# Kernel optimization log

Measured on AMD Instinct MI355X. Metric: run time of the kernel, lower is better.

## Reference

```python
import jax, jax.numpy as jnp
import numpy as np

B, N, D, H = 8, 128, 768, 64
NEG = -1e30
SLOPE = 0.01  # LeakyReLU slope
EPS = 1e-5    # BatchNorm eps


def setup_inputs() -> dict:
    key = jax.random.key(0)
    ks = jax.random.split(key, 10)
    s = 0.02
    feature = jax.random.normal(ks[0], (B, N, D), jnp.float32)
    aspect = jax.random.normal(ks[1], (B, D), jnp.float32)
    adj = jax.random.randint(ks[2], (B, N, N), 0, 2).astype(jnp.int32)
    W0 = jax.random.normal(ks[3], (D, D), jnp.float32) * s
    b0 = jnp.zeros((D,), jnp.float32)
    W1 = jax.random.normal(ks[4], (D, D), jnp.float32) * s
    b1 = jnp.zeros((D,), jnp.float32)
    A1 = jax.random.normal(ks[5], (2 * D, H), jnp.float32) * s  # afcs[0]
    ab1 = jnp.zeros((H,), jnp.float32)
    A2 = jax.random.normal(ks[6], (H, 1), jnp.float32) * s      # afcs[2]
    ab2 = jnp.zeros((1,), jnp.float32)
    gamma = jnp.ones((D,), jnp.float32)
    beta = jnp.zeros((D,), jnp.float32)
    return dict(feature=feature, aspect=aspect, adj=adj, W0=W0, b0=b0,
                W1=W1, b1=b1, A1=A1, ab1=ab1, A2=A2, ab2=ab2,
                gamma=gamma, beta=beta)


def reference(feature, aspect, adj, W0, b0, W1, b1, A1, ab1, A2, ab2, gamma, beta):
    # aspect is unused by the original forward.
    m = adj.astype(feature.dtype)          # [B,N,N] 0/1 mask
    d = A1.shape[0] // 2
    A1s, A1t = A1[:d], A1[d:]              # weight-split of Linear(2*mem_dim, H):
                                           # [h_i, h_j] @ A1 == h_i @ A1s + h_j @ A1t
    for (W, b) in ((W0, b0), (W1, b1)):
        h = feature @ W + b                # [B,N,D]
        s_src = h @ A1s                    # [B,N,H], broadcast over j
        s_tgt = h @ A1t                    # [B,N,H], broadcast over i
        hid = jax.nn.relu(s_src[:, :, None, :] + s_tgt[:, None, :, :] + ab1)  # [B,N,N,H]
        e = (hid @ A2)[..., 0] + ab2[0]    # [B,N,N]
        e = jnp.where(e > 0, e, SLOPE * e)  # LeakyReLU(0.01)
        logits = e * m + (1.0 - m) * NEG    # mask_logits
        b_, n_ = logits.shape[0], logits.shape[1]
        # NOTE: original softmaxes over the FLATTENED N*N axis, not per-row.
        attn = jax.nn.softmax(logits.reshape(b_, n_ * n_), axis=-1).reshape(b_, n_, n_)
        feature = jnp.einsum('bij,bjd->bid', attn, h)  # attention.bmm(h)
        # dropout is identity in eval / deterministic reference
    node_feature = feature
    g = node_feature.sum(axis=1)           # [B,D]
    mean = g.mean(axis=0)
    var = g.var(axis=0)                    # biased, matches BN training forward
    graph_feature = gamma * (g - mean) / jnp.sqrt(var + EPS) + beta
    return graph_feature, node_feature
```

## Files before the change

### kernel.cpp

```cpp
#include <hip/hip_runtime.h>
#include <math.h>

#define NEG_V (-1e30f)
#define SLOPE_V 0.01f
#define EPS_V 1e-5f

typedef __attribute__((ext_vector_type(8))) short bs8;
typedef __attribute__((ext_vector_type(4))) float f32x4;


__device__ __forceinline__ void split2(float x, unsigned short& hi, unsigned short& lo) {
    unsigned u = __float_as_uint(x);
    unsigned h = (u + 0x7FFFu + ((u >> 16) & 1u)) >> 16;
    hi = (unsigned short)h;
    float hf = __uint_as_float(h << 16);
    float l = x - hf;
    unsigned ul = __float_as_uint(l);
    lo = (unsigned short)((ul + 0x7FFFu + ((ul >> 16) & 1u)) >> 16);
}

#define MFMA_COMPUTE(B0)                                                       \
    {                                                                          \
        bs8 a_h[2], a_l[2], b_h[2], b_l[2];                                    \
        _Pragma("unroll")                                                      \
        for (int t = 0; t < 2; t++) {                                          \
            a_h[t] = *(bs8*)&buf[(B0) + 0][wm0 + t * 16 + lm][q * 8];          \
            a_l[t] = *(bs8*)&buf[(B0) + 1][wm0 + t * 16 + lm][q * 8];          \
            b_h[t] = *(bs8*)&buf[(B0) + 2][wn0 + t * 16 + lm][q * 8];          \
            b_l[t] = *(bs8*)&buf[(B0) + 3][wn0 + t * 16 + lm][q * 8];          \
        }                                                                      \
        _Pragma("unroll")                                                      \
        for (int mt = 0; mt < 2; mt++)                                         \
            _Pragma("unroll")                                                  \
            for (int nt = 0; nt < 2; nt++) {                                   \
                acc[mt][nt] = __builtin_amdgcn_mfma_f32_16x16x32_bf16(a_h[mt], b_h[nt], acc[mt][nt], 0, 0, 0); \
                acc[mt][nt] = __builtin_amdgcn_mfma_f32_16x16x32_bf16(a_h[mt], b_l[nt], acc[mt][nt], 0, 0, 0); \
                acc[mt][nt] = __builtin_amdgcn_mfma_f32_16x16x32_bf16(a_l[mt], b_h[nt], acc[mt][nt], 0, 0, 0); \
            }                                                                  \
    }

__device__ __forceinline__ void mfma_loop(
    const unsigned short* __restrict__ Ahg, const unsigned short* __restrict__ Alg,
    int lda,
    const unsigned short* __restrict__ Bhg, const unsigned short* __restrict__ Blg,
    int ldb, int K, int row0, int col0,
    f32x4 (&acc)[2][2],
    unsigned short (*buf)[64][40])
{
    const int tid = threadIdx.x;
    const int lane = tid & 63, wid = tid >> 6;
    const int wm0 = (wid >> 1) * 32, wn0 = (wid & 1) * 32;
    const int lm = lane & 15, q = lane >> 4;
    const int sr = tid >> 2, sc = (tid & 3) * 8;

    const unsigned short* pAh = Ahg + (size_t)(row0 + sr) * lda + sc;
    const unsigned short* pAl = Alg + (size_t)(row0 + sr) * lda + sc;
    const unsigned short* pBh = Bhg + (size_t)(col0 + sr) * ldb + sc;
    const unsigned short* pBl = Blg + (size_t)(col0 + sr) * ldb + sc;

    bs8 xAh = *(const bs8*)(pAh);
    bs8 xAl = *(const bs8*)(pAl);
    bs8 xBh = *(const bs8*)(pBh);
    bs8 xBl = *(const bs8*)(pBl);
    bs8 yAh = *(const bs8*)(pAh + 32);
    bs8 yAl = *(const bs8*)(pAl + 32);
    bs8 yBh = *(const bs8*)(pBh + 32);
    bs8 yBl = *(const bs8*)(pBl + 32);

    for (int k0 = 0; k0 < K; k0 += 64) {
        *(bs8*)&buf[0][sr][sc] = xAh;
        *(bs8*)&buf[1][sr][sc] = xAl;
        *(bs8*)&buf[2][sr][sc] = xBh;
        *(bs8*)&buf[3][sr][sc] = xBl;
        __syncthreads();
        if (k0 + 64 < K) {
            xAh = *(const bs8*)(pAh + k0 + 64);
            xAl = *(const bs8*)(pAl + k0 + 64);
            xBh = *(const bs8*)(pBh + k0 + 64);
            xBl = *(const bs8*)(pBl + k0 + 64);
        }
        MFMA_COMPUTE(0);
        *(bs8*)&buf[4][sr][sc] = yAh;
        *(bs8*)&buf[5][sr][sc] = yAl;
        *(bs8*)&buf[6][sr][sc] = yBh;
        *(bs8*)&buf[7][sr][sc] = yBl;
        __syncthreads();
        if (k0 + 96 < K) {
            yAh = *(const bs8*)(pAh + k0 + 96);
            yAl = *(const bs8*)(pAl + k0 + 96);
            yBh = *(const bs8*)(pBh + k0 + 96);
            yBl = *(const bs8*)(pBl + k0 + 96);
        }
        MFMA_COMPUTE(4);
    }
}

__device__ __forceinline__ void transpose_split_tile(
    const float* __restrict__ src, int src_ld,
    unsigned short* __restrict__ dh, unsigned short* __restrict__ dl, int dst_ld,
    unsigned short (*Th)[72], unsigned short (*Tl)[72])
{
    int tid = threadIdx.x;
    int r = tid >> 2;
    int cb = (tid & 3) * 16;
#pragma unroll
    for (int cc = 0; cc < 16; cc += 4) {
        float4 v = *(const float4*)(src + (size_t)r * src_ld + cb + cc);
        unsigned short hh, ll;
        split2(v.x, hh, ll); Th[cb + cc + 0][r] = hh; Tl[cb + cc + 0][r] = ll;
        split2(v.y, hh, ll); Th[cb + cc + 1][r] = hh; Tl[cb + cc + 1][r] = ll;
        split2(v.z, hh, ll); Th[cb + cc + 2][r] = hh; Tl[cb + cc + 2][r] = ll;
        split2(v.w, hh, ll); Th[cb + cc + 3][r] = hh; Tl[cb + cc + 3][r] = ll;
    }
    __syncthreads();
    int n = tid >> 2, ch = (tid & 3) * 8;
    *(bs8*)(dh + (size_t)n * dst_ld + ch)      = *(bs8*)&Th[n][ch];
    *(bs8*)(dh + (size_t)n * dst_ld + ch + 32) = *(bs8*)&Th[n][ch + 32];
    *(bs8*)(dl + (size_t)n * dst_ld + ch)      = *(bs8*)&Tl[n][ch];
    *(bs8*)(dl + (size_t)n * dst_ld + ch + 32) = *(bs8*)&Tl[n][ch + 32];
}

__device__ __forceinline__ void flat_split_job(
    const float* __restrict__ src, unsigned short* __restrict__ dh,
    unsigned short* __restrict__ dl, size_t base)
{
    unsigned short hh, ll;
#pragma unroll
    for (int g = 0; g < 2; g++) {
        bs8 sh, sl;
#pragma unroll
        for (int cc = 0; cc < 8; cc += 4) {
            float4 v = *(const float4*)(src + base + g * 8 + cc);
            split2(v.x, hh, ll); sh[cc + 0] = (short)hh; sl[cc + 0] = (short)ll;
            split2(v.y, hh, ll); sh[cc + 1] = (short)hh; sl[cc + 1] = (short)ll;
            split2(v.z, hh, ll); sh[cc + 2] = (short)hh; sl[cc + 2] = (short)ll;
            split2(v.w, hh, ll); sh[cc + 3] = (short)hh; sl[cc + 3] = (short)ll;
        }
        *(bs8*)(dh + base + g * 8) = sh;
        *(bs8*)(dl + base + g * 8) = sl;
    }
}

#define WA_STORE(va0, va1, vw0, vw1) {                                       \
    unsigned short hv, lv;                                                   \
    split2((va0).x, hv, lv); Ah[acs + 0][akk] = hv; Al[acs + 0][akk] = lv;   \
    split2((va0).y, hv, lv); Ah[acs + 1][akk] = hv; Al[acs + 1][akk] = lv;   \
    split2((va0).z, hv, lv); Ah[acs + 2][akk] = hv; Al[acs + 2][akk] = lv;   \
    split2((va0).w, hv, lv); Ah[acs + 3][akk] = hv; Al[acs + 3][akk] = lv;   \
    split2((va1).x, hv, lv); Ah[acs + 4][akk] = hv; Al[acs + 4][akk] = lv;   \
    split2((va1).y, hv, lv); Ah[acs + 5][akk] = hv; Al[acs + 5][akk] = lv;   \
    split2((va1).z, hv, lv); Ah[acs + 6][akk] = hv; Al[acs + 6][akk] = lv;   \
    split2((va1).w, hv, lv); Ah[acs + 7][akk] = hv; Al[acs + 7][akk] = lv;   \
    bs8 sh, sl;                                                              \
    split2((vw0).x, hv, lv); sh[0] = (short)hv; sl[0] = (short)lv;           \
    split2((vw0).y, hv, lv); sh[1] = (short)hv; sl[1] = (short)lv;           \
    split2((vw0).z, hv, lv); sh[2] = (short)hv; sl[2] = (short)lv;           \
    split2((vw0).w, hv, lv); sh[3] = (short)hv; sl[3] = (short)lv;           \
    split2((vw1).x, hv, lv); sh[4] = (short)hv; sl[4] = (short)lv;           \
    split2((vw1).y, hv, lv); sh[5] = (short)hv; sl[5] = (short)lv;           \
    split2((vw1).z, hv, lv); sh[6] = (short)hv; sl[6] = (short)lv;           \
    split2((vw1).w, hv, lv); sh[7] = (short)hv; sl[7] = (short)lv;           \
    *(bs8*)&Bh[br][bks] = sh;                                                \
    *(bs8*)&Bl[br][bks] = sl;                                                \
}

#define WA_FRAG() {                                                          \
    bs8 a_h[2], a_l[2], b_h[2], b_l[2];                                      \
    _Pragma("unroll")                                                        \
    for (int t = 0; t < 2; t++) {                                            \
        a_h[t] = *(bs8*)&Ah[wm0 + t * 16 + lm][q * 8];                       \
        a_l[t] = *(bs8*)&Al[wm0 + t * 16 + lm][q * 8];                       \
        b_h[t] = *(bs8*)&Bh[wn0 + t * 16 + lm][q * 8];                       \
        b_l[t] = *(bs8*)&Bl[wn0 + t * 16 + lm][q * 8];                       \
    }                                                                        \
    _Pragma("unroll")                                                        \
    for (int mt = 0; mt < 2; mt++)                                           \
        _Pragma("unroll")                                                    \
        for (int nt = 0; nt < 2; nt++) {                                     \
            acc[mt][nt] = __builtin_amdgcn_mfma_f32_16x16x32_bf16(a_h[mt], b_h[nt], acc[mt][nt], 0, 0, 0); \
            acc[mt][nt] = __builtin_amdgcn_mfma_f32_16x16x32_bf16(a_h[mt], b_l[nt], acc[mt][nt], 0, 0, 0); \
            acc[mt][nt] = __builtin_amdgcn_mfma_f32_16x16x32_bf16(a_l[mt], b_h[nt], acc[mt][nt], 0, 0, 0); \
        }                                                                    \
}

__global__ __launch_bounds__(256) void prep_k(
    const float* __restrict__ W0, const float* __restrict__ W1,
    const float* __restrict__ A1, const float* __restrict__ feature,
    const float* __restrict__ b0, const float* __restrict__ b1,
    unsigned short* Wt0h, unsigned short* Wt0l,
    unsigned short* Wt1h, unsigned short* Wt1l,
    unsigned short* fh, unsigned short* fl,
    unsigned short* WAth, unsigned short* WAtl,
    float* bA)
{
    __shared__ __align__(16) char smem[20480];
    int id = blockIdx.x, tid = threadIdx.x;
    if (id < 288) {
        unsigned short (*Th)[72] = (unsigned short(*)[72])(smem);
        unsigned short (*Tl)[72] = (unsigned short(*)[72])(smem + 9216);
        if (id < 144) {
            int kt = id / 12, nt = id % 12;
            transpose_split_tile(W0 + (size_t)(kt * 64) * 768 + nt * 64, 768,
                                 Wt0h + (size_t)(nt * 64) * 768 + kt * 64,
                                 Wt0l + (size_t)(nt * 64) * 768 + kt * 64, 768, Th, Tl);
        } else {
            int r = id - 144, kt = r / 12, nt = r % 12;
            transpose_split_tile(W1 + (size_t)(kt * 64) * 768 + nt * 64, 768,
                                 Wt1h + (size_t)(nt * 64) * 768 + kt * 64,
                                 Wt1l + (size_t)(nt * 64) * 768 + kt * 64, 768, Th, Tl);
        }
    } else if (id < 480) {
        flat_split_job(feature, fh, fl, (size_t)(id - 288) * 4096 + tid * 16);
    } else if (id < 528) {
        int j = id - 480;
        int c8 = j & 7, kq8 = j >> 3;
        int layer = (c8 >> 1) & 1;
        int ct = c8 & 1;
        int rt = kq8 + 6 * (c8 >> 2);
        const float* W = layer ? W1 : W0;
        const int r0 = rt * 64;
        unsigned short (*Ah)[40] = (unsigned short(*)[40])(smem);
        unsigned short (*Al)[40] = (unsigned short(*)[40])(smem + 5120);
        unsigned short (*Bh)[40] = (unsigned short(*)[40])(smem + 10240);
        unsigned short (*Bl)[40] = (unsigned short(*)[40])(smem + 15360);
        const int lane = tid & 63, wid = tid >> 6;
        const int wm0 = (wid >> 1) * 32, wn0 = (wid & 1) * 32;
        const int lm = lane & 15, q = lane >> 4;
        const int akk = tid & 31, acs = (tid >> 5) * 8;
        const int br = tid >> 2, bks = (tid & 3) * 8;
        const float* A1p = A1 + (size_t)(ct * 768 + akk) * 64 + acs;
        const float* Wp  = W + (size_t)(r0 + br) * 768 + bks;
        float4 xa0 = *(const float4*)(A1p);
        float4 xa1 = *(const float4*)(A1p + 4);
        float4 xw0 = *(const float4*)(Wp);
        float4 xw1 = *(const float4*)(Wp + 4);
        float4 ya0 = *(const float4*)(A1p + 32 * 64);
        float4 ya1 = *(const float4*)(A1p + 32 * 64 + 4);
        float4 yw0 = *(const float4*)(Wp + 32);
        float4 yw1 = *(const float4*)(Wp + 36);
        f32x4 acc[2][2] = {};
        for (int k0 = 0; k0 < 768; k0 += 64) {
            WA_STORE(xa0, xa1, xw0, xw1);
            __syncthreads();
            if (k0 + 64 < 768) {
                xa0 = *(const float4*)(A1p + (size_t)(k0 + 64) * 64);
                xa1 = *(const float4*)(A1p + (size_t)(k0 + 64) * 64 + 4);
                xw0 = *(const float4*)(Wp + k0 + 64);
                xw1 = *(const float4*)(Wp + k0 + 68);
            }
            WA_FRAG();
            __syncthreads();
            WA_STORE(ya0, ya1, yw0, yw1);
            __syncthreads();
            if (k0 + 96 < 768) {
                ya0 = *(const float4*)(A1p + (size_t)(k0 + 96) * 64);
                ya1 = *(const float4*)(A1p + (size_t)(k0 + 96) * 64 + 4);
                yw0 = *(const float4*)(Wp + k0 + 96);
                yw1 = *(const float4*)(Wp + k0 + 100);
            }
            WA_FRAG();
            __syncthreads();
        }
        const int c0 = ct * 64;
        size_t base = (size_t)layer * 98304;
#pragma unroll
        for (int mt = 0; mt < 2; mt++)
#pragma unroll
            for (int nt = 0; nt < 2; nt++) {
                int n = r0 + wn0 + nt * 16 + lm;
#pragma unroll
                for (int i = 0; i < 4; i++) {
                    int m = c0 + wm0 + mt * 16 + q * 4 + i;
                    unsigned short hv, lv;
                    split2(acc[mt][nt][i], hv, lv);
                    WAth[base + (size_t)m * 768 + n] = hv;
                    WAtl[base + (size_t)m * 768 + n] = lv;
                }
            }
    } else {
        float* redb = (float*)(smem);
        int layer = id - 528;
        const float* bv = layer ? b1 : b0;
        int c = tid & 127, half = tid >> 7;
        float acc = 0.f;
        for (int kk = 0; kk < 384; kk++) {
            int k = half * 384 + kk;
            int row = (c < 64 ? k : 768 + k);
            acc += bv[k] * A1[(size_t)row * 64 + (c & 63)];
        }
        redb[tid] = acc;
        __syncthreads();
        if (tid < 128) bA[layer * 128 + tid] = redb[tid] + redb[tid + 128];
    }
}

__global__ __launch_bounds__(256) void gemm_fused_k(
    const unsigned short* __restrict__ Ahg, const unsigned short* __restrict__ Alg,
    const unsigned short* __restrict__ Wth, const unsigned short* __restrict__ Wtl,
    const unsigned short* __restrict__ WAth, const unsigned short* __restrict__ WAtl,
    const float* __restrict__ bias,
    unsigned short* __restrict__ hth, unsigned short* __restrict__ htl,
    float* __restrict__ s)
{
    __shared__ unsigned short smem[8][64][40];
    int id = blockIdx.x;
    int g = id >> 3, r8 = id & 7;
    int hi2 = (g >= 14) ? 1 : 0;
    int by = r8 + 8 * hi2;
    int bx = g - 14 * hi2;
    int row0 = by * 64;
    const unsigned short* Bh;
    const unsigned short* Bl;
    int col0;
    if (bx < 12) { Bh = Wth;  Bl = Wtl;  col0 = bx * 64; }
    else         { Bh = WAth; Bl = WAtl; col0 = (bx - 12) * 64; }
    f32x4 acc[2][2] = {};
    mfma_loop(Ahg, Alg, 768, Bh, Bl, 768, 768, row0, col0, acc, smem);
    int tid = threadIdx.x, lane = tid & 63, wid = tid >> 6;
    int wm0 = (wid >> 1) * 32, wn0 = (wid & 1) * 32;
    int lm = lane & 15, q = lane >> 4;
    if (bx >= 12) {
#pragma unroll
        for (int mt = 0; mt < 2; mt++)
#pragma unroll
            for (int nt = 0; nt < 2; nt++) {
                int c = col0 + wn0 + nt * 16 + lm;
#pragma unroll
                for (int i = 0; i < 4; i++) {
                    int r = row0 + wm0 + mt * 16 + q * 4 + i;
                    s[(size_t)r * 128 + c] = acc[mt][nt][i];
                }
            }
        return;
    }
    __syncthreads();
    unsigned short* flat = &smem[0][0][0];
    unsigned short (*Hi)[69] = (unsigned short(*)[69])flat;
    unsigned short (*Lo)[69] = (unsigned short(*)[69])(flat + 4416);
#pragma unroll
    for (int mt = 0; mt < 2; mt++)
#pragma unroll
        for (int nt = 0; nt < 2; nt++) {
            int c = wn0 + nt * 16 + lm;
            float bv = bias[col0 + c];
#pragma unroll
            for (int i = 0; i < 4; i++) {
                int r = wm0 + mt * 16 + q * 4 + i;
                unsigned short hv, lv;
                split2(acc[mt][nt][i] + bv, hv, lv);
                Hi[r][c] = hv; Lo[r][c] = lv;
            }
        }
    __syncthreads();
    int d = tid >> 2, kq = (tid & 3) * 16;
    int b = row0 >> 7, kb = row0 & 127;
    bs8 th0, th1, tl0, tl1;
#pragma unroll
    for (int e = 0; e < 8; e++) {
        th0[e] = Hi[kq + e][d];     th1[e] = Hi[kq + 8 + e][d];
        tl0[e] = Lo[kq + e][d];     tl1[e] = Lo[kq + 8 + e][d];
    }
    size_t to = ((size_t)b * 768 + col0 + d) * 128 + kb + kq;
    *(bs8*)(hth + to) = th0; *(bs8*)(hth + to + 8) = th1;
    *(bs8*)(htl + to) = tl0; *(bs8*)(htl + to + 8) = tl1;
}

__global__ __launch_bounds__(256) void score_k(
    const float* __restrict__ s, const int* __restrict__ adj,
    const float* __restrict__ ab1, const float* __restrict__ A2,
    const float* __restrict__ ab2, const float* __restrict__ bA,
    unsigned short* __restrict__ ph, unsigned short* __restrict__ pl,
    float* __restrict__ psum)
{
    __shared__ float st[128][65];
    __shared__ float ss[4][65];
    __shared__ float a2s[64];
    __shared__ float warr[4];
    const int id = blockIdx.x, tid = threadIdx.x;
    const int b = id & 7, bx = id >> 3;
    const int i0 = bx * 4;
#pragma unroll
    for (int g = 0; g < 8; g++) {
        int idx4 = tid + g * 256;
        int j = idx4 >> 4;
        int h2 = (idx4 & 15) * 4;
        float4 v = *(const float4*)&s[(size_t)(b * 128 + j) * 128 + 64 + h2];
        float4 bv = *(const float4*)&bA[64 + h2];
        st[j][h2 + 0] = v.x + bv.x;
        st[j][h2 + 1] = v.y + bv.y;
        st[j][h2 + 2] = v.z + bv.z;
        st[j][h2 + 3] = v.w + bv.w;
    }
    {
        int i = tid >> 6, h2 = tid & 63;
        ss[i][h2] = s[(size_t)(b * 128 + i0 + i) * 128 + h2] + bA[h2] + ab1[h2];
    }
    if (tid < 64) a2s[tid] = A2[tid];
    __syncthreads();
    const float ab2v = ab2[0];
    const int rr = tid >> 7;
    const int j = tid & 127;
    const int r0 = rr * 2, r1 = rr * 2 + 1;
    float acc0 = 0.f, acc1 = 0.f;
#pragma unroll 4
    for (int h2 = 0; h2 < 64; h2++) {
        float bb = st[j][h2];
        float cv = a2s[h2];
        acc0 = fmaf(fmaxf(ss[r0][h2] + bb, 0.f), cv, acc0);
        acc1 = fmaf(fmaxf(ss[r1][h2] + bb, 0.f), cv, acc1);
    }
    float e0 = acc0 + ab2v; e0 = (e0 > 0.f) ? e0 : SLOPE_V * e0;
    float e1 = acc1 + ab2v; e1 = (e1 > 0.f) ? e1 : SLOPE_V * e1;
    size_t o0 = (size_t)b * 16384 + (size_t)(i0 + r0) * 128 + j;
    size_t o1 = (size_t)b * 16384 + (size_t)(i0 + r1) * 128 + j;
    float v0 = adj[o0] ? expf(e0) : 0.f;
    float v1 = adj[o1] ? expf(e1) : 0.f;
    unsigned short hv, lv;
    split2(v0, hv, lv); ph[o0] = hv; pl[o0] = lv;
    split2(v1, hv, lv); ph[o1] = hv; pl[o1] = lv;
    float vs = v0 + v1;
#pragma unroll
    for (int o = 32; o > 0; o >>= 1) vs += __shfl_down(vs, o);
    if ((tid & 63) == 0) warr[tid >> 6] = vs;
    __syncthreads();
    if (tid == 0) psum[b * 32 + bx] = warr[0] + warr[1] + warr[2] + warr[3];
}

__global__ __launch_bounds__(256) void attn_mfma_k(
    const unsigned short* __restrict__ ph, const unsigned short* __restrict__ pl,
    const unsigned short* __restrict__ hth, const unsigned short* __restrict__ htl,
    const float* __restrict__ psum, float* __restrict__ node,
    unsigned short* __restrict__ nodeh, unsigned short* __restrict__ nodel)
{
    __shared__ unsigned short smem[8][64][40];
    __shared__ float sred[33];
    int id = blockIdx.x;
    int b = id & 7, t = id >> 3;
    int cx = t % 12, ry = t / 12;
    int row0 = ry * 64, col0 = cx * 64;
    int tid = threadIdx.x;
    if (tid < 32) sred[tid] = psum[b * 32 + tid];
    __syncthreads();
    if (tid == 0) {
        float tt = 0.f;
#pragma unroll
        for (int i = 0; i < 32; i++) tt += sred[i];
        sred[32] = 1.0f / tt;
    }
    __syncthreads();
    float alpha = sred[32];
    f32x4 acc[2][2] = {};
    mfma_loop(ph + (size_t)b * 16384, pl + (size_t)b * 16384, 128,
              hth + (size_t)b * 98304, htl + (size_t)b * 98304, 128, 128,
              row0, col0, acc, smem);
    __syncthreads();
    float* C = node + (size_t)b * 98304;
    unsigned short* flat = &smem[0][0][0];
    unsigned short (*Hi)[69] = (unsigned short(*)[69])flat;
    unsigned short (*Lo)[69] = (unsigned short(*)[69])(flat + 4416);
    int lane = tid & 63, wid = tid >> 6;
    int wm0 = (wid >> 1) * 32, wn0 = (wid & 1) * 32;
    int lm = lane & 15, q = lane >> 4;
#pragma unroll
    for (int mt = 0; mt < 2; mt++)
#pragma unroll
        for (int nt = 0; nt < 2; nt++) {
            int c = wn0 + nt * 16 + lm;
#pragma unroll
            for (int i = 0; i < 4; i++) {
                int r = wm0 + mt * 16 + q * 4 + i;
                float v = acc[mt][nt][i] * alpha;
                C[(size_t)(row0 + r) * 768 + col0 + c] = v;
                unsigned short hv, lv;
                split2(v, hv, lv);
                Hi[r][c] = hv; Lo[r][c] = lv;
            }
        }
    __syncthreads();
    int r = tid >> 2, cq = (tid & 3) * 16;
    bs8 vh0, vh1, vl0, vl1;
#pragma unroll
    for (int e = 0; e < 8; e++) {
        vh0[e] = Hi[r][cq + e];     vh1[e] = Hi[r][cq + 8 + e];
        vl0[e] = Lo[r][cq + e];     vl1[e] = Lo[r][cq + 8 + e];
    }
    size_t ro = (size_t)(b * 128 + row0 + r) * 768 + col0 + cq;
    *(bs8*)(nodeh + ro) = vh0; *(bs8*)(nodeh + ro + 8) = vh1;
    *(bs8*)(nodel + ro) = vl0; *(bs8*)(nodel + ro + 8) = vl1;
}

__global__ __launch_bounds__(512) void gsum_bnorm_k(
    const float* __restrict__ node, const float* __restrict__ gamma,
    const float* __restrict__ beta, float* __restrict__ out)
{
    __shared__ float gbuf[8][64];
    __shared__ float mean_s[64], inv_s[64];
    int tid = threadIdx.x;
    int bg = tid >> 6, dl = tid & 63;
    int d = blockIdx.x * 64 + dl;
    const float* np = node + (size_t)(bg * 128) * 768 + d;
    float a0 = 0.f, a1 = 0.f, a2 = 0.f, a3 = 0.f;
#pragma unroll 4
    for (int i = 0; i < 128; i += 4) {
        a0 += np[(size_t)(i + 0) * 768];
        a1 += np[(size_t)(i + 1) * 768];
        a2 += np[(size_t)(i + 2) * 768];
        a3 += np[(size_t)(i + 3) * 768];
    }
    float v = (a0 + a1) + (a2 + a3);
    gbuf[bg][dl] = v;
    __syncthreads();
    if (tid < 64) {
        float m = 0.f;
#pragma unroll
        for (int b = 0; b < 8; b++) m += gbuf[b][tid];
        m *= 0.125f;
        float var = 0.f;
#pragma unroll
        for (int b = 0; b < 8; b++) { float t = gbuf[b][tid] - m; var += t * t; }
        var *= 0.125f;
        mean_s[tid] = m;
        inv_s[tid] = 1.0f / sqrtf(var + EPS_V);
    }
    __syncthreads();
    out[bg * 768 + d] = gamma[d] * (v - mean_s[dl]) * inv_s[dl] + beta[d];
}

extern "C" void kernel_launch(void* const* d_in, const int* in_sizes, int n_in,
                              void* d_out, int out_size, void* d_ws, size_t ws_size,
                              hipStream_t stream)
{
    const float* feature = (const float*)d_in[0];
    const int*   adj     = (const int*)d_in[2];
    const float* W0      = (const float*)d_in[3];
    const float* b0      = (const float*)d_in[4];
    const float* W1      = (const float*)d_in[5];
    const float* b1      = (const float*)d_in[6];
    const float* A1      = (const float*)d_in[7];
    const float* ab1     = (const float*)d_in[8];
    const float* A2      = (const float*)d_in[9];
    const float* ab2     = (const float*)d_in[10];
    const float* gamma   = (const float*)d_in[11];
    const float* beta    = (const float*)d_in[12];

    float* ws    = (float*)d_ws;
    float* s     = ws;
    float* psum  = ws + 131072;
    float* bA    = ws + 131328;
    unsigned short* u = (unsigned short*)(ws + 131584);
    unsigned short* Wt0h = u;
    unsigned short* Wt0l = Wt0h + 589824;
    unsigned short* Wt1h = Wt0l + 589824;
    unsigned short* Wt1l = Wt1h + 589824;
    unsigned short* WAth = Wt1l + 589824;
    unsigned short* WAtl = WAth + 196608;
    unsigned short* fh   = WAtl + 196608;
    unsigned short* fl   = fh + 786432;
    unsigned short* hth  = fl + 786432;
    unsigned short* htl  = hth + 786432;
    unsigned short* ndh  = htl + 786432;
    unsigned short* ndl  = ndh + 786432;
    unsigned short* ph   = ndl + 786432;
    unsigned short* pl   = ph + 131072;

    float* out       = (float*)d_out;
    float* graph_out = out;
    float* node_out  = out + 6144;

    prep_k<<<530, 256, 0, stream>>>(W0, W1, A1, feature, b0, b1,
                                    Wt0h, Wt0l, Wt1h, Wt1l,
                                    fh, fl, WAth, WAtl, bA);

    for (int layer = 0; layer < 2; layer++) {
        const unsigned short* Wth = layer ? Wt1h : Wt0h;
        const unsigned short* Wtl = layer ? Wt1l : Wt0l;
        const float* bb = layer ? b1 : b0;
        const unsigned short* Ahg = layer ? ndh : fh;
        const unsigned short* Alg = layer ? ndl : fl;
        gemm_fused_k<<<224, 256, 0, stream>>>(
            Ahg, Alg, Wth, Wtl, WAth + (size_t)layer * 98304,
            WAtl + (size_t)layer * 98304, bb, hth, htl, s);
        score_k<<<256, 256, 0, stream>>>(s, adj, ab1, A2, ab2,
                                         bA + layer * 128, ph, pl, psum);
        attn_mfma_k<<<192, 256, 0, stream>>>(ph, pl, hth, htl, psum,
                                             node_out, ndh, ndl);
    }
    gsum_bnorm_k<<<12, 512, 0, stream>>>(node_out, gamma, beta, graph_out);
}
```

Before: 157.2 us.

## Fuse graph column sums into attention epilogue and double-buffer prep WA GEMM

The per-batch node-feature column sums are now accumulated with atomics in the second-layer attention epilogue. score_k zeroes the accumulator, and a tiny bnorm kernel only normalizes, so node_out is no longer reread. The prep kernel's WA GEMM now uses two shared-memory buffers, which removes one barrier per half-iteration, and the attention kernel's psum reduction uses wave shuffles instead of shared memory plus barriers. In exchange the column sums depend on atomic ordering, so they are not bitwise deterministic, and prep_k uses twice the shared memory.

```diff
diff --git a/kernel.cpp b/kernel.cpp
--- a/kernel.cpp
+++ b/kernel.cpp
@@ -141,16 +141,16 @@
     }
 }
 
-#define WA_STORE(va0, va1, vw0, vw1) {                                       \
+#define WA_STORE(B0, va0, va1, vw0, vw1) {                                   \
     unsigned short hv, lv;                                                   \
-    split2((va0).x, hv, lv); Ah[acs + 0][akk] = hv; Al[acs + 0][akk] = lv;   \
-    split2((va0).y, hv, lv); Ah[acs + 1][akk] = hv; Al[acs + 1][akk] = lv;   \
-    split2((va0).z, hv, lv); Ah[acs + 2][akk] = hv; Al[acs + 2][akk] = lv;   \
-    split2((va0).w, hv, lv); Ah[acs + 3][akk] = hv; Al[acs + 3][akk] = lv;   \
-    split2((va1).x, hv, lv); Ah[acs + 4][akk] = hv; Al[acs + 4][akk] = lv;   \
-    split2((va1).y, hv, lv); Ah[acs + 5][akk] = hv; Al[acs + 5][akk] = lv;   \
-    split2((va1).z, hv, lv); Ah[acs + 6][akk] = hv; Al[acs + 6][akk] = lv;   \
-    split2((va1).w, hv, lv); Ah[acs + 7][akk] = hv; Al[acs + 7][akk] = lv;   \
+    split2((va0).x, hv, lv); buf[(B0)+0][acs + 0][akk] = hv; buf[(B0)+1][acs + 0][akk] = lv; \
+    split2((va0).y, hv, lv); buf[(B0)+0][acs + 1][akk] = hv; buf[(B0)+1][acs + 1][akk] = lv; \
+    split2((va0).z, hv, lv); buf[(B0)+0][acs + 2][akk] = hv; buf[(B0)+1][acs + 2][akk] = lv; \
+    split2((va0).w, hv, lv); buf[(B0)+0][acs + 3][akk] = hv; buf[(B0)+1][acs + 3][akk] = lv; \
+    split2((va1).x, hv, lv); buf[(B0)+0][acs + 4][akk] = hv; buf[(B0)+1][acs + 4][akk] = lv; \
+    split2((va1).y, hv, lv); buf[(B0)+0][acs + 5][akk] = hv; buf[(B0)+1][acs + 5][akk] = lv; \
+    split2((va1).z, hv, lv); buf[(B0)+0][acs + 6][akk] = hv; buf[(B0)+1][acs + 6][akk] = lv; \
+    split2((va1).w, hv, lv); buf[(B0)+0][acs + 7][akk] = hv; buf[(B0)+1][acs + 7][akk] = lv; \
     bs8 sh, sl;                                                              \
     split2((vw0).x, hv, lv); sh[0] = (short)hv; sl[0] = (short)lv;           \
     split2((vw0).y, hv, lv); sh[1] = (short)hv; sl[1] = (short)lv;           \
@@ -160,27 +160,8 @@
     split2((vw1).y, hv, lv); sh[5] = (short)hv; sl[5] = (short)lv;           \
     split2((vw1).z, hv, lv); sh[6] = (short)hv; sl[6] = (short)lv;           \
     split2((vw1).w, hv, lv); sh[7] = (short)hv; sl[7] = (short)lv;           \
-    *(bs8*)&Bh[br][bks] = sh;                                                \
-    *(bs8*)&Bl[br][bks] = sl;                                                \
-}
-
-#define WA_FRAG() {                                                          \
-    bs8 a_h[2], a_l[2], b_h[2], b_l[2];                                      \
-    _Pragma("unroll")                                                        \
-    for (int t = 0; t < 2; t++) {                                            \
-        a_h[t] = *(bs8*)&Ah[wm0 + t * 16 + lm][q * 8];                       \
-        a_l[t] = *(bs8*)&Al[wm0 + t * 16 + lm][q * 8];                       \
-        b_h[t] = *(bs8*)&Bh[wn0 + t * 16 + lm][q * 8];                       \
-        b_l[t] = *(bs8*)&Bl[wn0 + t * 16 + lm][q * 8];                       \
-    }                                                                        \
-    _Pragma("unroll")                                                        \
-    for (int mt = 0; mt < 2; mt++)                                           \
-        _Pragma("unroll")                                                    \
-        for (int nt = 0; nt < 2; nt++) {                                     \
-            acc[mt][nt] = __builtin_amdgcn_mfma_f32_16x16x32_bf16(a_h[mt], b_h[nt], acc[mt][nt], 0, 0, 0); \
-            acc[mt][nt] = __builtin_amdgcn_mfma_f32_16x16x32_bf16(a_h[mt], b_l[nt], acc[mt][nt], 0, 0, 0); \
-            acc[mt][nt] = __builtin_amdgcn_mfma_f32_16x16x32_bf16(a_l[mt], b_h[nt], acc[mt][nt], 0, 0, 0); \
-        }                                                                    \
+    *(bs8*)&buf[(B0)+2][br][bks] = sh;                                       \
+    *(bs8*)&buf[(B0)+3][br][bks] = sl;                                       \
 }
 
 __global__ __launch_bounds__(256) void prep_k(
@@ -193,7 +174,7 @@
     unsigned short* WAth, unsigned short* WAtl,
     float* bA)
 {
-    __shared__ __align__(16) char smem[20480];
+    __shared__ __align__(16) char smem[40960];
     int id = blockIdx.x, tid = threadIdx.x;
     if (id < 288) {
         unsigned short (*Th)[72] = (unsigned short(*)[72])(smem);
@@ -219,10 +200,7 @@
         int rt = kq8 + 6 * (c8 >> 2);
         const float* W = layer ? W1 : W0;
         const int r0 = rt * 64;
-        unsigned short (*Ah)[40] = (unsigned short(*)[40])(smem);
-        unsigned short (*Al)[40] = (unsigned short(*)[40])(smem + 5120);
-        unsigned short (*Bh)[40] = (unsigned short(*)[40])(smem + 10240);
-        unsigned short (*Bl)[40] = (unsigned short(*)[40])(smem + 15360);
+        unsigned short (*buf)[64][40] = (unsigned short(*)[64][40])smem;
         const int lane = tid & 63, wid = tid >> 6;
         const int wm0 = (wid >> 1) * 32, wn0 = (wid & 1) * 32;
         const int lm = lane & 15, q = lane >> 4;
@@ -240,7 +218,7 @@
         float4 yw1 = *(const float4*)(Wp + 36);
         f32x4 acc[2][2] = {};
         for (int k0 = 0; k0 < 768; k0 += 64) {
-            WA_STORE(xa0, xa1, xw0, xw1);
+            WA_STORE(0, xa0, xa1, xw0, xw1);
             __syncthreads();
             if (k0 + 64 < 768) {
                 xa0 = *(const float4*)(A1p + (size_t)(k0 + 64) * 64);
@@ -248,9 +226,8 @@
                 xw0 = *(const float4*)(Wp + k0 + 64);
                 xw1 = *(const float4*)(Wp + k0 + 68);
             }
-            WA_FRAG();
-            __syncthreads();
-            WA_STORE(ya0, ya1, yw0, yw1);
+            MFMA_COMPUTE(0);
+            WA_STORE(4, ya0, ya1, yw0, yw1);
             __syncthreads();
             if (k0 + 96 < 768) {
                 ya0 = *(const float4*)(A1p + (size_t)(k0 + 96) * 64);
@@ -258,8 +235,7 @@
                 yw0 = *(const float4*)(Wp + k0 + 96);
                 yw1 = *(const float4*)(Wp + k0 + 100);
             }
-            WA_FRAG();
-            __syncthreads();
+            MFMA_COMPUTE(4);
         }
         const int c0 = ct * 64;
         size_t base = (size_t)layer * 98304;
@@ -370,7 +346,7 @@
     const float* __restrict__ ab1, const float* __restrict__ A2,
     const float* __restrict__ ab2, const float* __restrict__ bA,
     unsigned short* __restrict__ ph, unsigned short* __restrict__ pl,
-    float* __restrict__ psum)
+    float* __restrict__ psum, float* __restrict__ g_ws)
 {
     __shared__ float st[128][65];
     __shared__ float ss[4][65];
@@ -379,6 +355,7 @@
     const int id = blockIdx.x, tid = threadIdx.x;
     const int b = id & 7, bx = id >> 3;
     const int i0 = bx * 4;
+    if (id < 24) g_ws[id * 256 + tid] = 0.f;
 #pragma unroll
     for (int g = 0; g < 8; g++) {
         int idx4 = tid + g * 256;
@@ -430,25 +407,19 @@
     const unsigned short* __restrict__ ph, const unsigned short* __restrict__ pl,
     const unsigned short* __restrict__ hth, const unsigned short* __restrict__ htl,
     const float* __restrict__ psum, float* __restrict__ node,
-    unsigned short* __restrict__ nodeh, unsigned short* __restrict__ nodel)
+    unsigned short* __restrict__ nodeh, unsigned short* __restrict__ nodel,
+    float* __restrict__ g_ws)
 {
     __shared__ unsigned short smem[8][64][40];
-    __shared__ float sred[33];
     int id = blockIdx.x;
     int b = id & 7, t = id >> 3;
     int cx = t % 12, ry = t / 12;
     int row0 = ry * 64, col0 = cx * 64;
     int tid = threadIdx.x;
-    if (tid < 32) sred[tid] = psum[b * 32 + tid];
-    __syncthreads();
-    if (tid == 0) {
-        float tt = 0.f;
-#pragma unroll
-        for (int i = 0; i < 32; i++) tt += sred[i];
-        sred[32] = 1.0f / tt;
-    }
-    __syncthreads();
-    float alpha = sred[32];
+    float pv = psum[b * 32 + (tid & 31)];
+#pragma unroll
+    for (int o = 1; o < 32; o <<= 1) pv += __shfl_xor(pv, o);
+    float alpha = 1.0f / pv;
     f32x4 acc[2][2] = {};
     mfma_loop(ph + (size_t)b * 16384, pl + (size_t)b * 16384, 128,
               hth + (size_t)b * 98304, htl + (size_t)b * 98304, 128, 128,
@@ -461,6 +432,7 @@
     int lane = tid & 63, wid = tid >> 6;
     int wm0 = (wid >> 1) * 32, wn0 = (wid & 1) * 32;
     int lm = lane & 15, q = lane >> 4;
+    float csum[2] = {0.f, 0.f};
 #pragma unroll
     for (int mt = 0; mt < 2; mt++)
 #pragma unroll
@@ -471,11 +443,17 @@
                 int r = wm0 + mt * 16 + q * 4 + i;
                 float v = acc[mt][nt][i] * alpha;
                 C[(size_t)(row0 + r) * 768 + col0 + c] = v;
+                csum[nt] += v;
                 unsigned short hv, lv;
                 split2(v, hv, lv);
                 Hi[r][c] = hv; Lo[r][c] = lv;
             }
         }
+    if (g_ws) {
+#pragma unroll
+        for (int nt = 0; nt < 2; nt++)
+            atomicAdd(&g_ws[b * 768 + col0 + wn0 + nt * 16 + lm], csum[nt]);
+    }
     __syncthreads();
     int r = tid >> 2, cq = (tid & 3) * 16;
     bs8 vh0, vh1, vl0, vl1;
@@ -489,41 +467,24 @@
     *(bs8*)(nodel + ro) = vl0; *(bs8*)(nodel + ro + 8) = vl1;
 }
 
-__global__ __launch_bounds__(512) void gsum_bnorm_k(
-    const float* __restrict__ node, const float* __restrict__ gamma,
+__global__ __launch_bounds__(64) void bnorm_k(
+    const float* __restrict__ g_ws, const float* __restrict__ gamma,
     const float* __restrict__ beta, float* __restrict__ out)
 {
-    __shared__ float gbuf[8][64];
-    __shared__ float mean_s[64], inv_s[64];
-    int tid = threadIdx.x;
-    int bg = tid >> 6, dl = tid & 63;
-    int d = blockIdx.x * 64 + dl;
-    const float* np = node + (size_t)(bg * 128) * 768 + d;
-    float a0 = 0.f, a1 = 0.f, a2 = 0.f, a3 = 0.f;
-#pragma unroll 4
-    for (int i = 0; i < 128; i += 4) {
-        a0 += np[(size_t)(i + 0) * 768];
-        a1 += np[(size_t)(i + 1) * 768];
-        a2 += np[(size_t)(i + 2) * 768];
-        a3 += np[(size_t)(i + 3) * 768];
-    }
-    float v = (a0 + a1) + (a2 + a3);
-    gbuf[bg][dl] = v;
-    __syncthreads();
-    if (tid < 64) {
-        float m = 0.f;
-#pragma unroll
-        for (int b = 0; b < 8; b++) m += gbuf[b][tid];
-        m *= 0.125f;
-        float var = 0.f;
-#pragma unroll
-        for (int b = 0; b < 8; b++) { float t = gbuf[b][tid] - m; var += t * t; }
-        var *= 0.125f;
-        mean_s[tid] = m;
-        inv_s[tid] = 1.0f / sqrtf(var + EPS_V);
-    }
-    __syncthreads();
-    out[bg * 768 + d] = gamma[d] * (v - mean_s[dl]) * inv_s[dl] + beta[d];
+    int d = blockIdx.x * 64 + threadIdx.x;
+    float vals[8]; float m = 0.f;
+#pragma unroll
+    for (int b = 0; b < 8; b++) { vals[b] = g_ws[b * 768 + d]; m += vals[b]; }
+    m *= 0.125f;
+    float var = 0.f;
+#pragma unroll
+    for (int b = 0; b < 8; b++) { float t = vals[b] - m; var += t * t; }
+    var *= 0.125f;
+    float inv = 1.0f / sqrtf(var + EPS_V);
+    float gm = gamma[d], bt = beta[d];
+#pragma unroll
+    for (int b = 0; b < 8; b++)
+        out[b * 768 + d] = gm * (vals[b] - m) * inv + bt;
 }
 
 extern "C" void kernel_launch(void* const* d_in, const int* in_sizes, int n_in,
@@ -547,7 +508,8 @@
     float* s     = ws;
     float* psum  = ws + 131072;
     float* bA    = ws + 131328;
-    unsigned short* u = (unsigned short*)(ws + 131584);
+    float* g_ws  = ws + 131584;
+    unsigned short* u = (unsigned short*)(ws + 137728);
     unsigned short* Wt0h = u;
     unsigned short* Wt0l = Wt0h + 589824;
     unsigned short* Wt1h = Wt0l + 589824;
@@ -581,9 +543,10 @@
             Ahg, Alg, Wth, Wtl, WAth + (size_t)layer * 98304,
             WAtl + (size_t)layer * 98304, bb, hth, htl, s);
         score_k<<<256, 256, 0, stream>>>(s, adj, ab1, A2, ab2,
-                                         bA + layer * 128, ph, pl, psum);
+                                         bA + layer * 128, ph, pl, psum, g_ws);
         attn_mfma_k<<<192, 256, 0, stream>>>(ph, pl, hth, htl, psum,
-                                             node_out, ndh, ndl);
-    }
-    gsum_bnorm_k<<<12, 512, 0, stream>>>(node_out, gamma, beta, graph_out);
-}
+                                             node_out, ndh, ndl,
+                                             layer ? g_ws : (float*)nullptr);
+    }
+    bnorm_k<<<12, 64, 0, stream>>>(g_ws, gamma, beta, graph_out);
+}
```

Result: faster. 149.9 us (-4.7%).
